# Performance work log

Hardware: AMD Instinct MI355X
Metric: run time of the kernel (lower is better)

## Reference

```python
import jax, jax.numpy as jnp
import numpy as np

D_MODEL, D_STATE, D_CONV, EXPAND = 512, 16, 4, 2
D_INNER = EXPAND * D_MODEL
DT_RANK = D_MODEL // 16
B, N = 4, 576


def layernorm(x, g, b, eps=1e-5):
    m = x.mean(-1, keepdims=True)
    v = jnp.mean((x - m) ** 2, axis=-1, keepdims=True)
    return (x - m) / jnp.sqrt(v + eps) * g + b


def selective_scan(u, dt, A, Bm, Cm, Dp):
    # u, dt: (B,N,di); Bm,Cm: (B,N,ds); A: (di,ds); Dp: (di,)
    dA = jnp.exp(dt[..., None] * A)                      # (B,N,di,ds)
    dBu = dt[..., None] * Bm[:, :, None, :] * u[..., None]

    def step(h, inp):
        dA_t, dBu_t, C_t = inp                            # (B,di,ds),(B,di,ds),(B,ds)
        h = dA_t * h + dBu_t
        y = jnp.einsum('bds,bs->bd', h, C_t)
        return h, y

    h0 = jnp.zeros((u.shape[0], u.shape[2], A.shape[1]), u.dtype)
    _, ys = jax.lax.scan(step, h0, (dA.transpose(1, 0, 2, 3),
                                    dBu.transpose(1, 0, 2, 3),
                                    Cm.transpose(1, 0, 2)))
    return ys.transpose(1, 0, 2) + u * Dp


def mamba(x, Win, convw, convb, Wx, Wdt, bdt, Alog, Dp, Wout):
    xz = jnp.einsum('bnd,ed->bne', x, Win)                # (B,N,2*di)
    u, z = jnp.split(xz, 2, axis=-1)
    k = convw.shape[1]
    # depthwise causal conv1d
    uc = jax.lax.conv_general_dilated(u.transpose(0, 2, 1), convw[:, None, :],
                                      (1,), [(k - 1, 0)],
                                      feature_group_count=convw.shape[0])
    u = jax.nn.silu((uc + convb[None, :, None]).transpose(0, 2, 1))
    x_dbl = jnp.einsum('bnd,ed->bne', u, Wx)              # (B,N,dt_rank+2*ds)
    ds = Alog.shape[1]
    dt, Bm, Cm = jnp.split(x_dbl, [DT_RANK, DT_RANK + ds], axis=-1)
    dt = jax.nn.softplus(jnp.einsum('bnr,dr->bnd', dt, Wdt) + bdt)
    A = -jnp.exp(Alog)
    y = selective_scan(u, dt, A, Bm, Cm, Dp)
    y = y * jax.nn.silu(z)
    return jnp.einsum('bnd,ed->bne', y, Wout)


def setup_inputs() -> dict:
    key = jax.random.key(0)
    ks = iter(jax.random.split(key, 40))
    s = 0.02
    def rn(shape, scale=s):
        return jax.random.normal(next(ks), shape, jnp.float32) * scale
    inp = {
        'x': jax.random.normal(next(ks), (B, N, D_MODEL), jnp.float32),
        'g1': jnp.ones((D_MODEL,), jnp.float32), 'b1': jnp.zeros((D_MODEL,), jnp.float32),
        'g2': jnp.ones((D_MODEL,), jnp.float32), 'b2': jnp.zeros((D_MODEL,), jnp.float32),
        'merge_W': rn((D_MODEL, 2 * D_MODEL)), 'merge_b': jnp.zeros((D_MODEL,), jnp.float32),
        'ffn_W1': rn((4 * D_MODEL, D_MODEL)), 'ffn_b1': jnp.zeros((4 * D_MODEL,), jnp.float32),
        'ffn_W2': rn((D_MODEL, 4 * D_MODEL)), 'ffn_b2': jnp.zeros((D_MODEL,), jnp.float32),
    }
    for p in ('f_', 'r_'):
        inp[p + 'Win'] = rn((2 * D_INNER, D_MODEL))
        inp[p + 'convw'] = rn((D_INNER, D_CONV), 0.1)
        inp[p + 'convb'] = jnp.zeros((D_INNER,), jnp.float32)
        inp[p + 'Wx'] = rn((DT_RANK + 2 * D_STATE, D_INNER))
        inp[p + 'Wdt'] = rn((D_INNER, DT_RANK), 0.1)
        inp[p + 'bdt'] = jnp.zeros((D_INNER,), jnp.float32)
        inp[p + 'Alog'] = jnp.log(jnp.broadcast_to(jnp.arange(1, D_STATE + 1, dtype=jnp.float32), (D_INNER, D_STATE)))
        inp[p + 'D'] = jnp.ones((D_INNER,), jnp.float32)
        inp[p + 'Wout'] = rn((D_MODEL, D_INNER))
    return inp


def reference(x, g1, b1, g2, b2,
              f_Win, f_convw, f_convb, f_Wx, f_Wdt, f_bdt, f_Alog, f_D, f_Wout,
              r_Win, r_convw, r_convb, r_Wx, r_Wdt, r_bdt, r_Alog, r_D, r_Wout,
              merge_W, merge_b, ffn_W1, ffn_b1, ffn_W2, ffn_b2):
    residual = x
    xn = layernorm(x, g1, b1)
    xf = mamba(xn, f_Win, f_convw, f_convb, f_Wx, f_Wdt, f_bdt, f_Alog, f_D, f_Wout)
    xb = mamba(jnp.flip(xn, axis=1), r_Win, r_convw, r_convb, r_Wx, r_Wdt, r_bdt, r_Alog, r_D, r_Wout)
    xb = jnp.flip(xb, axis=1)
    xm = jnp.concatenate([xf, xb], axis=-1)
    xm = jnp.einsum('bne,de->bnd', xm, merge_W) + merge_b
    x = residual + xm  # dropout is identity in eval mode
    residual = x
    xn = layernorm(x, g2, b2)
    h = jax.nn.gelu(jnp.einsum('bnd,ed->bne', xn, ffn_W1) + ffn_b1)
    h = jnp.einsum('bne,de->bnd', h, ffn_W2) + ffn_b2
    return residual + h
```

## Files before the change

### kernel.cpp

```cpp
#include <hip/hip_runtime.h>
#include <hip/hip_bf16.h>
#include <math.h>

#define D_MODEL 512
#define D_STATE 16
#define D_CONV  4
#define D_INNER 1024
#define DT_RANK 32
#define BB      4
#define NN      576
#define TOK     (BB*NN)

__device__ __forceinline__ float fexp(float x)  { return __expf(x); }
__device__ __forceinline__ float fsilu(float x) { return x / (1.f + __expf(-x)); }
__device__ __forceinline__ float fsoftplus(float x) {
    return fmaxf(x, 0.f) + __logf(1.f + __expf(-fabsf(x)));
}
__device__ __forceinline__ float fgelu(float u) {
    float a = 0.7978845608028654f * (u + 0.044715f * u * u * u);
    float t = 1.f - 2.f / (1.f + __expf(2.f * a));
    return 0.5f * u * (1.f + t);
}

__global__ __launch_bounds__(64) void ln_kernel(const float* __restrict__ x,
                                                const float* __restrict__ g,
                                                const float* __restrict__ b,
                                                float* __restrict__ o) {
    int t = blockIdx.x;
    int lane = threadIdx.x;
    const float* xr = x + (size_t)t * D_MODEL;
    float4 v0 = ((const float4*)xr)[lane];
    float4 v1 = ((const float4*)xr)[64 + lane];
    float s = v0.x + v0.y + v0.z + v0.w + v1.x + v1.y + v1.z + v1.w;
    #pragma unroll
    for (int m = 32; m; m >>= 1) s += __shfl_xor(s, m);
    float mean = s * (1.0f / D_MODEL);
    float dx[8] = {v0.x-mean, v0.y-mean, v0.z-mean, v0.w-mean,
                   v1.x-mean, v1.y-mean, v1.z-mean, v1.w-mean};
    float q = 0.f;
    #pragma unroll
    for (int i = 0; i < 8; i++) q += dx[i]*dx[i];
    #pragma unroll
    for (int m = 32; m; m >>= 1) q += __shfl_xor(q, m);
    float rstd = rsqrtf(q * (1.0f / D_MODEL) + 1e-5f);
    float4 g0 = ((const float4*)g)[lane], g1 = ((const float4*)g)[64 + lane];
    float4 b0 = ((const float4*)b)[lane], b1 = ((const float4*)b)[64 + lane];
    float4 o0, o1;
    o0.x = dx[0]*rstd*g0.x + b0.x; o0.y = dx[1]*rstd*g0.y + b0.y;
    o0.z = dx[2]*rstd*g0.z + b0.z; o0.w = dx[3]*rstd*g0.w + b0.w;
    o1.x = dx[4]*rstd*g1.x + b1.x; o1.y = dx[5]*rstd*g1.y + b1.y;
    o1.z = dx[6]*rstd*g1.z + b1.z; o1.w = dx[7]*rstd*g1.w + b1.w;
    float* orow = o + (size_t)t * D_MODEL;
    ((float4*)orow)[lane] = o0;
    ((float4*)orow)[64 + lane] = o1;
}

#define EP_NONE     0
#define EP_SOFTPLUS 1
#define EP_GELU     2
#define EP_BIAS_ADD 3

typedef __attribute__((ext_vector_type(8))) short bf16x8;
typedef __attribute__((ext_vector_type(4))) float f32x4;

__device__ __forceinline__ void split8(float4 q0, float4 q1,
                                       uint4 &hi, uint4 &lo) {
    float f[8] = {q0.x, q0.y, q0.z, q0.w, q1.x, q1.y, q1.z, q1.w};
    unsigned hb[8], lb[8];
    #pragma unroll
    for (int i = 0; i < 8; i++) {
        unsigned u = __float_as_uint(f[i]);
        unsigned r = (u + 0x7FFFu + ((u >> 16) & 1u)) >> 16;
        hb[i] = r & 0xFFFFu;
        float lf = f[i] - __uint_as_float(r << 16);
        unsigned ul = __float_as_uint(lf);
        lb[i] = ((ul + 0x7FFFu + ((ul >> 16) & 1u)) >> 16) & 0xFFFFu;
    }
    hi = make_uint4(hb[0]|(hb[1]<<16), hb[2]|(hb[3]<<16),
                    hb[4]|(hb[5]<<16), hb[6]|(hb[7]<<16));
    lo = make_uint4(lb[0]|(lb[1]<<16), lb[2]|(lb[3]<<16),
                    lb[4]|(lb[5]<<16), lb[6]|(lb[7]<<16));
}

template<int EP>
__global__ __launch_bounds__(256) void gemm_mfma(
        const float* __restrict__ A, int lda,
        const float* __restrict__ W,
        float* __restrict__ C, int ldc,
        const float* __restrict__ bias,
        const float* __restrict__ add, int ldadd,
        int N, int K) {
    __shared__ short AsH[64][40], AsL[64][40], BsH[64][40], BsL[64][40];
    int tid  = threadIdx.x;
    int lane = tid & 63;
    int wave = tid >> 6;
    int wm = wave >> 1, wn = wave & 1;
    int m0 = blockIdx.y * 64, n0 = blockIdx.x * 64;
    int srow = tid >> 2;
    int skb  = (tid & 3) * 8;

    f32x4 acc[2][2] = {};

    for (int k0 = 0; k0 < K; k0 += 32) {
        float4 a0 = *(const float4*)&A[(size_t)(m0 + srow) * lda + k0 + skb];
        float4 a1 = *(const float4*)&A[(size_t)(m0 + srow) * lda + k0 + skb + 4];
        float4 w0 = *(const float4*)&W[(size_t)(n0 + srow) * K + k0 + skb];
        float4 w1 = *(const float4*)&W[(size_t)(n0 + srow) * K + k0 + skb + 4];
        uint4 ah, al, bh, bl;
        split8(a0, a1, ah, al);
        split8(w0, w1, bh, bl);
        __syncthreads();
        *(uint4*)&AsH[srow][skb] = ah;
        *(uint4*)&AsL[srow][skb] = al;
        *(uint4*)&BsH[srow][skb] = bh;
        *(uint4*)&BsL[srow][skb] = bl;
        __syncthreads();

        int hk = (lane >> 4) * 8;
        int rr = lane & 15;
        bf16x8 fAh[2], fAl[2], fBh[2], fBl[2];
        #pragma unroll
        for (int mi = 0; mi < 2; mi++) {
            int r = wm * 32 + mi * 16 + rr;
            fAh[mi] = *(const bf16x8*)&AsH[r][hk];
            fAl[mi] = *(const bf16x8*)&AsL[r][hk];
        }
        #pragma unroll
        for (int ni = 0; ni < 2; ni++) {
            int c = wn * 32 + ni * 16 + rr;
            fBh[ni] = *(const bf16x8*)&BsH[c][hk];
            fBl[ni] = *(const bf16x8*)&BsL[c][hk];
        }
        #pragma unroll
        for (int mi = 0; mi < 2; mi++)
            #pragma unroll
            for (int ni = 0; ni < 2; ni++) {
                acc[mi][ni] = __builtin_amdgcn_mfma_f32_16x16x32_bf16(
                    fAh[mi], fBh[ni], acc[mi][ni], 0, 0, 0);
                acc[mi][ni] = __builtin_amdgcn_mfma_f32_16x16x32_bf16(
                    fAh[mi], fBl[ni], acc[mi][ni], 0, 0, 0);
                acc[mi][ni] = __builtin_amdgcn_mfma_f32_16x16x32_bf16(
                    fAl[mi], fBh[ni], acc[mi][ni], 0, 0, 0);
            }
    }

    #pragma unroll
    for (int mi = 0; mi < 2; mi++) {
        #pragma unroll
        for (int ni = 0; ni < 2; ni++) {
            int r0 = m0 + wm * 32 + mi * 16 + (lane >> 4) * 4;
            int c  = n0 + wn * 32 + ni * 16 + (lane & 15);
            #pragma unroll
            for (int j = 0; j < 4; j++) {
                float v = acc[mi][ni][j];
                if (EP == EP_GELU) {
                    v = fgelu(v + bias[c]);
                } else if (EP == EP_BIAS_ADD) {
                    v += bias[c];
                    v += add[(size_t)(r0 + j) * ldadd + c];
                }
                C[(size_t)(r0 + j) * ldc + c] = v;
            }
        }
    }
}

template<int EP>
__global__ __launch_bounds__(256) void gemm_nt(
        const float* __restrict__ A, int lda,
        const float* __restrict__ W,
        float* __restrict__ C, int ldc,
        const float* __restrict__ bias,
        const float* __restrict__ add, int ldadd,
        int M, int N, int K) {
    __shared__ float As[32][68];
    __shared__ float Bs[32][68];
    int tid = threadIdx.x;
    int tx = tid & 15, ty = tid >> 4;
    int m0 = blockIdx.y * 64, n0 = blockIdx.x * 64;
    int arow = tid >> 3;
    int acol = (tid & 7) * 4;
    float acc[4][4] = {};

    for (int k0 = 0; k0 < K; k0 += 32) {
        float4 a0 = *(const float4*)&A[(size_t)(m0 + arow) * lda + k0 + acol];
        float4 a1 = *(const float4*)&A[(size_t)(m0 + arow + 32) * lda + k0 + acol];
        float4 w0 = *(const float4*)&W[(size_t)(n0 + arow) * K + k0 + acol];
        float4 w1 = *(const float4*)&W[(size_t)(n0 + arow + 32) * K + k0 + acol];
        __syncthreads();
        As[acol + 0][arow] = a0.x; As[acol + 1][arow] = a0.y;
        As[acol + 2][arow] = a0.z; As[acol + 3][arow] = a0.w;
        As[acol + 0][arow + 32] = a1.x; As[acol + 1][arow + 32] = a1.y;
        As[acol + 2][arow + 32] = a1.z; As[acol + 3][arow + 32] = a1.w;
        Bs[acol + 0][arow] = w0.x; Bs[acol + 1][arow] = w0.y;
        Bs[acol + 2][arow] = w0.z; Bs[acol + 3][arow] = w0.w;
        Bs[acol + 0][arow + 32] = w1.x; Bs[acol + 1][arow + 32] = w1.y;
        Bs[acol + 2][arow + 32] = w1.z; Bs[acol + 3][arow + 32] = w1.w;
        __syncthreads();
        #pragma unroll
        for (int kk = 0; kk < 32; kk++) {
            float av[4], bv[4];
            *(float4*)&av[0] = *(const float4*)&As[kk][ty * 4];
            *(float4*)&bv[0] = *(const float4*)&Bs[kk][tx * 4];
            #pragma unroll
            for (int i = 0; i < 4; i++)
                #pragma unroll
                for (int j = 0; j < 4; j++)
                    acc[i][j] = fmaf(av[i], bv[j], acc[i][j]);
        }
    }

    int mbase = m0 + ty * 4, nbase = n0 + tx * 4;
    #pragma unroll
    for (int i = 0; i < 4; i++) {
        float vv[4];
        #pragma unroll
        for (int j = 0; j < 4; j++) {
            float v = acc[i][j];
            if (EP == EP_SOFTPLUS) {
                v = fsoftplus(v + bias[nbase + j]);
            } else if (EP == EP_GELU) {
                v = fgelu(v + bias[nbase + j]);
            } else if (EP == EP_BIAS_ADD) {
                v += bias[nbase + j];
                v += add[(size_t)(mbase + i) * ldadd + nbase + j];
            }
            vv[j] = v;
        }
        *(float4*)&C[(size_t)(mbase + i) * ldc + nbase] =
            make_float4(vv[0], vv[1], vv[2], vv[3]);
    }
}

__global__ __launch_bounds__(256) void gemm_wx_splitk(
        const float* __restrict__ A,
        const float* __restrict__ W,
        float* __restrict__ Cpart) {
    __shared__ float As[32][68];
    __shared__ float Bs[32][68];
    int tid = threadIdx.x;
    int tx = tid & 15, ty = tid >> 4;
    int m0 = blockIdx.y * 64;
    int z = blockIdx.z;
    const float* Az = A + z * 256;
    const float* Wz = W + z * 256;
    int arow = tid >> 3;
    int acol = (tid & 7) * 4;
    float acc[4][4] = {};

    for (int k0 = 0; k0 < 256; k0 += 32) {
        float4 a0 = *(const float4*)&Az[(size_t)(m0 + arow) * 1024 + k0 + acol];
        float4 a1 = *(const float4*)&Az[(size_t)(m0 + arow + 32) * 1024 + k0 + acol];
        float4 w0 = *(const float4*)&Wz[(size_t)(arow) * 1024 + k0 + acol];
        float4 w1 = *(const float4*)&Wz[(size_t)(arow + 32) * 1024 + k0 + acol];
        __syncthreads();
        As[acol + 0][arow] = a0.x; As[acol + 1][arow] = a0.y;
        As[acol + 2][arow] = a0.z; As[acol + 3][arow] = a0.w;
        As[acol + 0][arow + 32] = a1.x; As[acol + 1][arow + 32] = a1.y;
        As[acol + 2][arow + 32] = a1.z; As[acol + 3][arow + 32] = a1.w;
        Bs[acol + 0][arow] = w0.x; Bs[acol + 1][arow] = w0.y;
        Bs[acol + 2][arow] = w0.z; Bs[acol + 3][arow] = w0.w;
        Bs[acol + 0][arow + 32] = w1.x; Bs[acol + 1][arow + 32] = w1.y;
        Bs[acol + 2][arow + 32] = w1.z; Bs[acol + 3][arow + 32] = w1.w;
        __syncthreads();
        #pragma unroll
        for (int kk = 0; kk < 32; kk++) {
            float av[4], bv[4];
            *(float4*)&av[0] = *(const float4*)&As[kk][ty * 4];
            *(float4*)&bv[0] = *(const float4*)&Bs[kk][tx * 4];
            #pragma unroll
            for (int i = 0; i < 4; i++)
                #pragma unroll
                for (int j = 0; j < 4; j++)
                    acc[i][j] = fmaf(av[i], bv[j], acc[i][j]);
        }
    }

    float* Cz = Cpart + (size_t)z * TOK * 64;
    int mbase = m0 + ty * 4, nbase = tx * 4;
    #pragma unroll
    for (int i = 0; i < 4; i++)
        *(float4*)&Cz[(size_t)(mbase + i) * 64 + nbase] =
            make_float4(acc[i][0], acc[i][1], acc[i][2], acc[i][3]);
}

__global__ __launch_bounds__(256) void reduce4_kernel(
        const float* __restrict__ Cpart, float* __restrict__ xd) {
    int i = blockIdx.x * 256 + threadIdx.x;
    const int M64 = TOK * 64;
    xd[i] = Cpart[i] + Cpart[M64 + i] + Cpart[2 * M64 + i] + Cpart[3 * M64 + i];
}

__global__ __launch_bounds__(256) void conv_silu_kernel(
        const float* __restrict__ xz, const float* __restrict__ w,
        const float* __restrict__ cb, float* __restrict__ out, int dir) {
    int idx = blockIdx.x * 256 + threadIdx.x;
    int c = idx & (D_INNER - 1);
    int t = idx >> 10;
    int b = t / NN, n = t % NN;
    const float* up = xz + (size_t)b * NN * (2 * D_INNER) + c;
    float4 wv = *(const float4*)&w[c * 4];
    float acc;
    if (dir == 0) {
        acc =                 up[(size_t)n * (2*D_INNER)] * wv.w;
        if (n >= 1) acc = fmaf(up[(size_t)(n-1) * (2*D_INNER)], wv.z, acc);
        if (n >= 2) acc = fmaf(up[(size_t)(n-2) * (2*D_INNER)], wv.y, acc);
        if (n >= 3) acc = fmaf(up[(size_t)(n-3) * (2*D_INNER)], wv.x, acc);
    } else {
        acc =                    up[(size_t)n * (2*D_INNER)] * wv.w;
        if (n+1 < NN) acc = fmaf(up[(size_t)(n+1) * (2*D_INNER)], wv.z, acc);
        if (n+2 < NN) acc = fmaf(up[(size_t)(n+2) * (2*D_INNER)], wv.y, acc);
        if (n+3 < NN) acc = fmaf(up[(size_t)(n+3) * (2*D_INNER)], wv.x, acc);
    }
    out[(size_t)t * D_INNER + c] = fsilu(acc + cb[c]);
}

__global__ __launch_bounds__(256) void scan_kernel(
        const float* __restrict__ dt, const float* __restrict__ xdbl,
        const float* __restrict__ u, const float* __restrict__ xz,
        const float* __restrict__ Alog, const float* __restrict__ Dp,
        float* __restrict__ y, int dir) {
    int lane = threadIdx.x & 63;
    int wave = threadIdx.x >> 6;
    int w = blockIdx.x * 4 + wave;
    int s = lane & 15;
    int dl = lane >> 4;
    int b = w >> 8;
    int d = (w & 255) * 4 + dl;
    float A_ds = -fexp(Alog[d * D_STATE + s]);
    float Dd = Dp[d];
    float h = 0.f;
    const int UF = 16;
    for (int i0 = 0; i0 < NN; i0 += UF) {
        float dtv[UF], uv[UF], Bv[UF], Cv[UF];
        #pragma unroll
        for (int j = 0; j < UF; j++) {
            int i = i0 + j;
            int n = dir ? (NN - 1 - i) : i;
            size_t tt = (size_t)b * NN + n;
            dtv[j] = dt[tt * D_INNER + d];
            uv[j]  = u[tt * D_INNER + d];
            Bv[j]  = xdbl[tt * 64 + 32 + s];
            Cv[j]  = xdbl[tt * 64 + 48 + s];
        }
        float p[UF];
        #pragma unroll
        for (int j = 0; j < UF; j++) {
            float dA = fexp(dtv[j] * A_ds);
            h = fmaf(dA, h, dtv[j] * Bv[j] * uv[j]);
            p[j] = h * Cv[j];
        }
        #pragma unroll
        for (int j = 0; j < UF; j++) {
            p[j] += __shfl_xor(p[j], 1);
            p[j] += __shfl_xor(p[j], 2);
            p[j] += __shfl_xor(p[j], 4);
            p[j] += __shfl_xor(p[j], 8);
        }
        if (s == 0) {
            #pragma unroll
            for (int j = 0; j < UF; j++) {
                int i = i0 + j;
                int n = dir ? (NN - 1 - i) : i;
                size_t tt = (size_t)b * NN + n;
                float zv = xz[tt * (2 * D_INNER) + D_INNER + d];
                float yv = p[j] + uv[j] * Dd;
                yv *= fsilu(zv);
                y[tt * D_INNER + d] = yv;
            }
        }
    }
}

extern "C" void kernel_launch(void* const* d_in, const int* in_sizes, int n_in,
                              void* d_out, int out_size, void* d_ws, size_t ws_size,
                              hipStream_t stream) {
    const float* x       = (const float*)d_in[0];
    const float* g1      = (const float*)d_in[1];
    const float* b1      = (const float*)d_in[2];
    const float* g2      = (const float*)d_in[3];
    const float* b2      = (const float*)d_in[4];
    const float* merge_W = (const float*)d_in[5];
    const float* merge_b = (const float*)d_in[6];
    const float* ffn_W1  = (const float*)d_in[7];
    const float* ffn_b1  = (const float*)d_in[8];
    const float* ffn_W2  = (const float*)d_in[9];
    const float* ffn_b2  = (const float*)d_in[10];
    const float* Win[2]   = {(const float*)d_in[11], (const float*)d_in[20]};
    const float* convw[2] = {(const float*)d_in[12], (const float*)d_in[21]};
    const float* convb[2] = {(const float*)d_in[13], (const float*)d_in[22]};
    const float* Wx[2]    = {(const float*)d_in[14], (const float*)d_in[23]};
    const float* Wdt[2]   = {(const float*)d_in[15], (const float*)d_in[24]};
    const float* bdt[2]   = {(const float*)d_in[16], (const float*)d_in[25]};
    const float* Alog[2]  = {(const float*)d_in[17], (const float*)d_in[26]};
    const float* Dp[2]    = {(const float*)d_in[18], (const float*)d_in[27]};
    const float* Wout[2]  = {(const float*)d_in[19], (const float*)d_in[28]};
    float* out = (float*)d_out;

    float* ws = (float*)d_ws;
    const size_t T = TOK;
    float* xn  = ws;
    float* xz  = xn  + T * 512;
    float* uc  = xz  + T * 2048;
    float* xd  = uc  + T * 1024;
    float* dt  = xd  + T * 64;
    float* xfb = dt  + T * 1024;
    float* x2  = xfb + T * 1024;
    float* xd4 = x2;

    ln_kernel<<<TOK, 64, 0, stream>>>(x, g1, b1, xn);

    for (int p = 0; p < 2; p++) {
        gemm_mfma<EP_NONE><<<dim3(2048/64, TOK/64), 256, 0, stream>>>(
            xn, 512, Win[p], xz, 2048, nullptr, nullptr, 0, 2048, 512);
        conv_silu_kernel<<<TOK * D_INNER / 256, 256, 0, stream>>>(
            xz, convw[p], convb[p], uc, p);
        gemm_wx_splitk<<<dim3(1, TOK/64, 4), 256, 0, stream>>>(uc, Wx[p], xd4);
        reduce4_kernel<<<TOK * 64 / 256, 256, 0, stream>>>(xd4, xd);
        gemm_nt<EP_SOFTPLUS><<<dim3(1024/64, TOK/64), 256, 0, stream>>>(
            xd, 64, Wdt[p], dt, 1024, bdt[p], nullptr, 0, TOK, 1024, 32);
        scan_kernel<<<256, 256, 0, stream>>>(
            dt, xd, uc, xz, Alog[p], Dp[p], uc, p);
        gemm_mfma<EP_NONE><<<dim3(512/64, TOK/64), 256, 0, stream>>>(
            uc, 1024, Wout[p], xfb + p * 512, 1024, nullptr, nullptr, 0, 512, 1024);
    }

    gemm_mfma<EP_BIAS_ADD><<<dim3(512/64, TOK/64), 256, 0, stream>>>(
        xfb, 1024, merge_W, x2, 512, merge_b, x, 512, 512, 1024);

    ln_kernel<<<TOK, 64, 0, stream>>>(x2, g2, b2, xn);

    gemm_mfma<EP_GELU><<<dim3(2048/64, TOK/64), 256, 0, stream>>>(
        xn, 512, ffn_W1, xz, 2048, ffn_b1, nullptr, 0, 2048, 512);

    gemm_mfma<EP_BIAS_ADD><<<dim3(512/64, TOK/64), 256, 0, stream>>>(
        xz, 2048, ffn_W2, out, 512, ffn_b2, x2, 512, 512, 2048);
}
```

Baseline: 671.2 us.

## Split selective scan into chunked three-pass parallel scan

Replaces the single sequential scan kernel with a chunked scan over 6 sequence chunks. Pass one computes each chunk's end state and cumulative decay product, a combine kernel propagates carry-in states across chunks, and pass two reruns each chunk from its carry-in to produce outputs. This raises the grid from 256 blocks to 1536 so the GPU has more parallel work to hide the long serial dependency chain. In exchange the recurrence is computed twice, there are two extra launches, and intermediates are written to scratch space aliased onto x2.

```diff
diff --git a/kernel.cpp b/kernel.cpp
--- a/kernel.cpp
+++ b/kernel.cpp
@@ -10,6 +10,8 @@
 #define BB      4
 #define NN      576
 #define TOK     (BB*NN)
+#define NCHUNK  6
+#define CLEN    (NN/NCHUNK)
 
 __device__ __forceinline__ float fexp(float x)  { return __expf(x); }
 __device__ __forceinline__ float fsilu(float x) { return x / (1.f + __expf(-x)); }
@@ -315,23 +317,76 @@
     out[(size_t)t * D_INNER + c] = fsilu(acc + cb[c]);
 }
 
-__global__ __launch_bounds__(256) void scan_kernel(
+__global__ __launch_bounds__(256) void scan_pass1(
         const float* __restrict__ dt, const float* __restrict__ xdbl,
-        const float* __restrict__ u, const float* __restrict__ xz,
-        const float* __restrict__ Alog, const float* __restrict__ Dp,
-        float* __restrict__ y, int dir) {
+        const float* __restrict__ u, const float* __restrict__ Alog,
+        float* __restrict__ hend, float* __restrict__ prodA, int dir) {
     int lane = threadIdx.x & 63;
     int wave = threadIdx.x >> 6;
     int w = blockIdx.x * 4 + wave;
     int s = lane & 15;
     int dl = lane >> 4;
-    int b = w >> 8;
-    int d = (w & 255) * 4 + dl;
+    int dg = w & 255;
+    int b  = (w >> 8) & 3;
+    int c  = w >> 10;
+    int d = dg * 4 + dl;
+    float A_ds = -fexp(Alog[d * D_STATE + s]);
+    float h = 0.f, P = 1.f;
+    const int UF = 16;
+    for (int i0 = c * CLEN; i0 < (c + 1) * CLEN; i0 += UF) {
+        float dtv[UF], uv[UF], Bv[UF];
+        #pragma unroll
+        for (int j = 0; j < UF; j++) {
+            int i = i0 + j;
+            int n = dir ? (NN - 1 - i) : i;
+            size_t tt = (size_t)b * NN + n;
+            dtv[j] = dt[tt * D_INNER + d];
+            uv[j]  = u[tt * D_INNER + d];
+            Bv[j]  = xdbl[tt * 64 + 32 + s];
+        }
+        #pragma unroll
+        for (int j = 0; j < UF; j++) {
+            float a = fexp(dtv[j] * A_ds);
+            h = fmaf(a, h, dtv[j] * Bv[j] * uv[j]);
+            P *= a;
+        }
+    }
+    int idx = ((c * 4 + b) * 1024 + d) * 16 + s;
+    hend[idx] = h;
+    prodA[idx] = P;
+}
+
+__global__ __launch_bounds__(256) void scan_combine(
+        const float* __restrict__ hend, const float* __restrict__ prodA,
+        float* __restrict__ hin) {
+    int e = blockIdx.x * 256 + threadIdx.x;
+    float run = 0.f;
+    #pragma unroll
+    for (int c = 0; c < NCHUNK; c++) {
+        hin[c * 65536 + e] = run;
+        run = fmaf(prodA[c * 65536 + e], run, hend[c * 65536 + e]);
+    }
+}
+
+__global__ __launch_bounds__(256) void scan_pass2(
+        const float* __restrict__ dt, const float* __restrict__ xdbl,
+        const float* __restrict__ u, const float* __restrict__ xz,
+        const float* __restrict__ Alog, const float* __restrict__ Dp,
+        const float* __restrict__ hin, float* __restrict__ y, int dir) {
+    int lane = threadIdx.x & 63;
+    int wave = threadIdx.x >> 6;
+    int w = blockIdx.x * 4 + wave;
+    int s = lane & 15;
+    int dl = lane >> 4;
+    int dg = w & 255;
+    int b  = (w >> 8) & 3;
+    int c  = w >> 10;
+    int d = dg * 4 + dl;
     float A_ds = -fexp(Alog[d * D_STATE + s]);
     float Dd = Dp[d];
-    float h = 0.f;
+    float h = hin[((c * 4 + b) * 1024 + d) * 16 + s];
     const int UF = 16;
-    for (int i0 = 0; i0 < NN; i0 += UF) {
+    for (int i0 = c * CLEN; i0 < (c + 1) * CLEN; i0 += UF) {
         float dtv[UF], uv[UF], Bv[UF], Cv[UF];
         #pragma unroll
         for (int j = 0; j < UF; j++) {
@@ -346,8 +401,8 @@
         float p[UF];
         #pragma unroll
         for (int j = 0; j < UF; j++) {
-            float dA = fexp(dtv[j] * A_ds);
-            h = fmaf(dA, h, dtv[j] * Bv[j] * uv[j]);
+            float a = fexp(dtv[j] * A_ds);
+            h = fmaf(a, h, dtv[j] * Bv[j] * uv[j]);
             p[j] = h * Cv[j];
         }
         #pragma unroll
@@ -406,7 +461,10 @@
     float* dt  = xd  + T * 64;
     float* xfb = dt  + T * 1024;
     float* x2  = xfb + T * 1024;
-    float* xd4 = x2;
+    float* xd4   = x2;
+    float* hendb = x2;
+    float* prodb = x2 + (size_t)NCHUNK * 65536;
+    float* hinb  = x2 + (size_t)2 * NCHUNK * 65536;
 
     ln_kernel<<<TOK, 64, 0, stream>>>(x, g1, b1, xn);
 
@@ -419,8 +477,11 @@
         reduce4_kernel<<<TOK * 64 / 256, 256, 0, stream>>>(xd4, xd);
         gemm_nt<EP_SOFTPLUS><<<dim3(1024/64, TOK/64), 256, 0, stream>>>(
             xd, 64, Wdt[p], dt, 1024, bdt[p], nullptr, 0, TOK, 1024, 32);
-        scan_kernel<<<256, 256, 0, stream>>>(
-            dt, xd, uc, xz, Alog[p], Dp[p], uc, p);
+        scan_pass1<<<NCHUNK * 256, 256, 0, stream>>>(
+            dt, xd, uc, Alog[p], hendb, prodb, p);
+        scan_combine<<<256, 256, 0, stream>>>(hendb, prodb, hinb);
+        scan_pass2<<<NCHUNK * 256, 256, 0, stream>>>(
+            dt, xd, uc, xz, Alog[p], Dp[p], hinb, uc, p);
         gemm_mfma<EP_NONE><<<dim3(512/64, TOK/64), 256, 0, stream>>>(
             uc, 1024, Wout[p], xfb + p * 512, 1024, nullptr, nullptr, 0, 512, 1024);
     }
```

Result: faster. 595.0 us (-11.4%).
